# Performance work log

Hardware: AMD Instinct MI355X
Metric: run time of the kernel (lower is better)

## Reference

```python
import jax, jax.numpy as jnp
import numpy as np

T, B, I, Hd = 512, 64, 1024, 2048


def setup_inputs() -> dict:
    key = jax.random.key(0)
    ks = jax.random.split(key, 10)
    s_in = 1.0 / np.sqrt(I)
    s_h = 1.0 / np.sqrt(Hd)
    return {
        "inputs": jax.random.normal(ks[0], (T, B, I), jnp.float32),
        "state": jax.random.normal(ks[1], (B, Hd), jnp.float32),
        "W_xz": jax.random.normal(ks[2], (I, Hd), jnp.float32) * s_in,
        "W_hz": jax.random.normal(ks[3], (Hd, Hd), jnp.float32) * s_h,
        "b_z": jnp.zeros((Hd,), jnp.float32),
        "W_xr": jax.random.normal(ks[4], (I, Hd), jnp.float32) * s_in,
        "W_hr": jax.random.normal(ks[5], (Hd, Hd), jnp.float32) * s_h,
        "b_r": jnp.zeros((Hd,), jnp.float32),
        "W_xh": jax.random.normal(ks[6], (I, Hd), jnp.float32) * s_in,
        "W_hh": jax.random.normal(ks[7], (Hd, Hd), jnp.float32) * s_h,
        "b_h": jnp.zeros((Hd,), jnp.float32),
        "W_hq": jax.random.normal(ks[8], (Hd, I), jnp.float32) * s_h,
        "b_hq": jnp.zeros((I,), jnp.float32),
    }


def reference(inputs, state, W_xz, W_hz, b_z, W_xr, W_hr, b_r,
              W_xh, W_hh, b_h, W_hq, b_hq):
    def step(H, X):
        Z = jax.nn.sigmoid(X @ W_xz + H @ W_hz + b_z)
        R = jax.nn.sigmoid(X @ W_xr + H @ W_hr + b_r)
        # torch `R * H @ W_hh` parses left-to-right: (R*H) @ W_hh
        H_tilda = jnp.tanh(X @ W_xh + (R * H) @ W_hh + b_h)
        H_new = Z * H + (1.0 - Z) * H_tilda
        Y = H_new @ W_hq + b_hq
        return H_new, Y

    H_final, Ys = jax.lax.scan(step, state, inputs)  # Ys: (T, B, I)
    out = Ys.reshape(-1, Ys.shape[-1])  # torch.cat(output, dim=0) -> (T*B, I)
    return out, H_final
```

## Files before the change

### kernel.cpp

```cpp
#include <hip/hip_runtime.h>
#include <cstdint>
#include <cstddef>


#define T_ 512
#define B_ 64
#define I_ 1024
#define H_ 2048
#define NB 256
#define NTHREADS 512
#define GSTRIDE (NB * NTHREADS)

typedef __attribute__((ext_vector_type(8))) __bf16 bf16x8;
typedef __attribute__((ext_vector_type(2))) __bf16 bf16x2;
typedef __attribute__((ext_vector_type(4))) float f32x4;
typedef __attribute__((ext_vector_type(2))) float f32x2;

static constexpr unsigned SMEM_BYTES = 128 * 1024 + 20 * 1024;

static constexpr size_t OFF_SLOT = 0;
static constexpr size_t OFF_HNF  = 16384;
static constexpr size_t OFF_RHF  = 24576;
static constexpr size_t OFF_XF   = 32768;
static constexpr size_t OFF_WXZT = 36864;
static constexpr size_t SZ_WXT   = (size_t)H_ * I_ * 2;
static constexpr size_t SZ_WHT   = (size_t)H_ * H_ * 2;
static constexpr size_t OFF_WXRT = OFF_WXZT + SZ_WXT;
static constexpr size_t OFF_WXHT = OFF_WXRT + SZ_WXT;
static constexpr size_t OFF_WHZT = OFF_WXHT + SZ_WXT;
static constexpr size_t OFF_WHRT = OFF_WHZT + SZ_WHT;
static constexpr size_t OFF_WHHT = OFF_WHRT + SZ_WHT;
static constexpr size_t OFF_WHQT = OFF_WHHT + SZ_WHT;
static constexpr size_t OFF_XBF  = OFF_WHQT + SZ_WXT;
static constexpr size_t OFF_HBF  = OFF_XBF + (size_t)2 * B_ * I_ * 2;
static constexpr size_t OFF_RHBF = OFF_HBF + (size_t)2 * B_ * H_ * 2;
static constexpr size_t WS_NEEDED = OFF_RHBF + (size_t)B_ * H_ * 2;

__device__ __forceinline__ float fsigmoid(float x) { return 1.0f / (1.0f + __expf(-x)); }
__device__ __forceinline__ float ftanh(float x)    { return 2.0f / (1.0f + __expf(-2.0f * x)) - 1.0f; }

__device__ __forceinline__ void cstore8(void* p, unsigned long long v) {
    __hip_atomic_store((unsigned long long*)p, v, __ATOMIC_RELAXED, __HIP_MEMORY_SCOPE_AGENT);
}
__device__ __forceinline__ void cstore4(void* p, unsigned v) {
    __hip_atomic_store((unsigned*)p, v, __ATOMIC_RELAXED, __HIP_MEMORY_SCOPE_AGENT);
}
__device__ __forceinline__ void fstore(unsigned* p, unsigned v) {
    __hip_atomic_store(p, v, __ATOMIC_RELAXED, __HIP_MEMORY_SCOPE_AGENT);
}
__device__ __forceinline__ unsigned long long pack4bf(float a, float b, float c, float d) {
    union { unsigned short s[4]; unsigned long long u; } x;
    union { __bf16 b; unsigned short s; } t;
    t.b = (__bf16)a; x.s[0] = t.s;
    t.b = (__bf16)b; x.s[1] = t.s;
    t.b = (__bf16)c; x.s[2] = t.s;
    t.b = (__bf16)d; x.s[3] = t.s;
    return x.u;
}
__device__ __forceinline__ unsigned pack2bf(float a, float b) {
    union { unsigned short s[2]; unsigned u; } x;
    union { __bf16 b; unsigned short s; } t;
    t.b = (__bf16)a; x.s[0] = t.s;
    t.b = (__bf16)b; x.s[1] = t.s;
    return x.u;
}

template<int NFLAGS>
__device__ __forceinline__ void flag_wait(unsigned* flags, unsigned want) {
    const int tid = (int)threadIdx.x;
    if (tid < NFLAGS) {
        while (__hip_atomic_load(&flags[tid * 16], __ATOMIC_RELAXED,
                                 __HIP_MEMORY_SCOPE_AGENT) < want)
            __builtin_amdgcn_s_sleep(1);
    }
    __syncthreads();
    if (tid == 0)
        (void)__hip_atomic_load(&flags[0], __ATOMIC_ACQUIRE, __HIP_MEMORY_SCOPE_AGENT);
    __syncthreads();
    asm volatile("" ::: "memory");
}

__device__ __forceinline__ void transpose_cvt(const float* __restrict__ src,
                                              __bf16* __restrict__ dst,
                                              int K, int lgN) {
    const int N = 1 << lgN;
    const int total = K << lgN;
    for (int idx = (int)(blockIdx.x * blockDim.x + threadIdx.x); idx < total; idx += GSTRIDE) {
        int k = idx >> lgN;
        int n = idx & (N - 1);
        dst[(size_t)n * K + k] = (__bf16)src[idx];
    }
}

__device__ __forceinline__ void gload16(const void* g, void* l) {
    __builtin_amdgcn_global_load_lds(
        (const __attribute__((address_space(1))) unsigned int*)g,
        (__attribute__((address_space(3))) unsigned int*)l,
        16, 0, 0);
}

#define STAGE_SEG(i)                                                          \
    do {                                                                      \
        const int kb_ = (w + ((i) << 3)) << 5;                                \
        char* slot_ = wls + (((i) & 3) << 12);                                \
        _Pragma("unroll")                                                     \
        for (int c_ = 0; c_ < 4; ++c_) {                                      \
            const int row_ = (c_ << 4) + (lane >> 2);                         \
            const int jl_ = (lane & 3) ^ ((row_ >> 1) & 3);                   \
            gload16(A + (size_t)row_ * ks + kb_ + (jl_ << 3),                 \
                    slot_ + (c_ << 10));                                      \
        }                                                                     \
    } while (0)

#define WAITV(rem)                                                            \
    do {                                                                      \
        if ((rem) >= 3)      asm volatile("s_waitcnt vmcnt(12)" ::: "memory");\
        else if ((rem) == 2) asm volatile("s_waitcnt vmcnt(8)" ::: "memory"); \
        else if ((rem) == 1) asm volatile("s_waitcnt vmcnt(4)" ::: "memory"); \
        else                 asm volatile("s_waitcnt vmcnt(0)" ::: "memory"); \
        __builtin_amdgcn_sched_barrier(0);                                    \
    } while (0)

template<int NSEG, int OFF, int N>
__device__ __forceinline__ void gemm_lds1(
    const __bf16* __restrict__ A, int ks, const bf16x8 (&pb)[N],
    f32x4 acc[4], char* __restrict__ wls)
{
    static_assert(OFF + NSEG <= N, "frags");
    const int tid  = (int)threadIdx.x;
    const int lane = tid & 63;
    const int w    = tid >> 6;
    const int l15  = lane & 15;

    asm volatile("s_waitcnt lgkmcnt(0)" ::: "memory");
    __builtin_amdgcn_sched_barrier(0);
    STAGE_SEG(0);
    if constexpr (NSEG > 1) STAGE_SEG(1);
    if constexpr (NSEG > 2) STAGE_SEG(2);
    if constexpr (NSEG > 3) STAGE_SEG(3);
#pragma unroll
    for (int i = 0; i < NSEG; ++i) {
        WAITV(NSEG - 1 - i);
        const char* slot = wls + ((i & 3) << 12);
        bf16x8 pa[4];
#pragma unroll
        for (int m = 0; m < 4; ++m) {
            const int row = (m << 4) + l15;
            const int j   = (lane >> 4) ^ ((row >> 1) & 3);
            pa[m] = *(const bf16x8*)(slot + row * 64 + (j << 4));
        }
#pragma unroll
        for (int m = 0; m < 4; ++m)
            acc[m] = __builtin_amdgcn_mfma_f32_16x16x32_bf16(pa[m], pb[OFF + i], acc[m], 0, 0, 0);
        if (i + 4 < NSEG) {
            asm volatile("s_waitcnt lgkmcnt(0)" ::: "memory");
            __builtin_amdgcn_sched_barrier(0);
            STAGE_SEG(i + 4);
        }
    }
}

template<int N1, int N2>
__device__ __forceinline__ void gemm_lds2(
    const __bf16* __restrict__ A, int ks,
    const bf16x8 (&pb1)[N1], const bf16x8 (&pb2)[N2],
    f32x4 a1[4], f32x4 a2[4], char* __restrict__ wls)
{
    const int tid  = (int)threadIdx.x;
    const int lane = tid & 63;
    const int w    = tid >> 6;
    const int l15  = lane & 15;

    asm volatile("s_waitcnt lgkmcnt(0)" ::: "memory");
    __builtin_amdgcn_sched_barrier(0);
    STAGE_SEG(0); STAGE_SEG(1); STAGE_SEG(2); STAGE_SEG(3);
#pragma unroll
    for (int i = 0; i < 4; ++i) {
        WAITV(3 - i);
        const char* slot = wls + ((i & 3) << 12);
        bf16x8 pa[4];
#pragma unroll
        for (int m = 0; m < 4; ++m) {
            const int row = (m << 4) + l15;
            const int j   = (lane >> 4) ^ ((row >> 1) & 3);
            pa[m] = *(const bf16x8*)(slot + row * 64 + (j << 4));
        }
#pragma unroll
        for (int m = 0; m < 4; ++m) {
            a1[m] = __builtin_amdgcn_mfma_f32_16x16x32_bf16(pa[m], pb1[i], a1[m], 0, 0, 0);
            a2[m] = __builtin_amdgcn_mfma_f32_16x16x32_bf16(pa[m], pb2[i], a2[m], 0, 0, 0);
        }
    }
}

__device__ __forceinline__ void gemm_reduce(f32x4 acc[4], float* __restrict__ red,
                                            float out2[2]) {
    constexpr int RP = 20;
    const int tid  = (int)threadIdx.x;
    const int lane = tid & 63;
    const int w    = tid >> 6;
    const int l15  = lane & 15;
    const int q4   = (lane >> 4) << 2;

    if (w >= 4) {
        float* rw = red + (size_t)(w - 4) * (64 * RP);
#pragma unroll
        for (int m = 0; m < 4; ++m)
#pragma unroll
            for (int r = 0; r < 4; ++r)
                rw[((m << 4) + q4 + r) * RP + l15] = acc[m][r];
    }
    __syncthreads();
    if (w < 4) {
        float* rw = red + (size_t)w * (64 * RP);
#pragma unroll
        for (int m = 0; m < 4; ++m)
#pragma unroll
            for (int r = 0; r < 4; ++r)
                rw[((m << 4) + q4 + r) * RP + l15] += acc[m][r];
    }
    __syncthreads();
    {
        const int a = (tid >> 3) * RP + ((tid & 7) << 1);
        f32x2 s0 = *(const f32x2*)(red + a);
        f32x2 s1 = *(const f32x2*)(red + 64 * RP + a);
        f32x2 s2 = *(const f32x2*)(red + 2 * 64 * RP + a);
        f32x2 s3 = *(const f32x2*)(red + 3 * 64 * RP + a);
        f32x2 s = s0 + s1 + s2 + s3;
        out2[0] = s[0]; out2[1] = s[1];
    }
}

__global__ __launch_bounds__(NTHREADS, 2)
__attribute__((amdgpu_waves_per_eu(2, 2)))
void gru_persistent(
    const float* __restrict__ inputs, const float* __restrict__ state,
    const float* __restrict__ Wxz, const float* __restrict__ Whz, const float* __restrict__ bz,
    const float* __restrict__ Wxr, const float* __restrict__ Whr, const float* __restrict__ br,
    const float* __restrict__ Wxh, const float* __restrict__ Whh, const float* __restrict__ bh,
    const float* __restrict__ Whq, const float* __restrict__ bhq,
    float* __restrict__ out, char* __restrict__ ws) {

    unsigned* slots = (unsigned*)(ws + OFF_SLOT);
    unsigned* hnf   = (unsigned*)(ws + OFF_HNF);
    unsigned* rhf   = (unsigned*)(ws + OFF_RHF);
    unsigned* xf    = (unsigned*)(ws + OFF_XF);
    __bf16* WxzT = (__bf16*)(ws + OFF_WXZT);
    __bf16* WxrT = (__bf16*)(ws + OFF_WXRT);
    __bf16* WxhT = (__bf16*)(ws + OFF_WXHT);
    __bf16* WhzT = (__bf16*)(ws + OFF_WHZT);
    __bf16* WhrT = (__bf16*)(ws + OFF_WHRT);
    __bf16* WhhT = (__bf16*)(ws + OFF_WHHT);
    __bf16* WhqT = (__bf16*)(ws + OFF_WHQT);
    __bf16* Xbf  = (__bf16*)(ws + OFF_XBF);
    __bf16* Hbf  = (__bf16*)(ws + OFF_HBF);
    __bf16* RHbf = (__bf16*)(ws + OFF_RHBF);

    extern __shared__ char smem[];
    char* wls  = smem + ((threadIdx.x >> 6) << 14);
    float* red = (float*)(smem + 128 * 1024);

    const int b   = (int)blockIdx.x;
    const int tid = (int)threadIdx.x;
    const int c16 = (b & 127) << 4;
    const int gr  = tid >> 3;
    const int gc  = (tid & 7) << 1;

    transpose_cvt(Wxz, WxzT, I_, 11);
    transpose_cvt(Wxr, WxrT, I_, 11);
    transpose_cvt(Wxh, WxhT, I_, 11);
    transpose_cvt(Whz, WhzT, H_, 11);
    transpose_cvt(Whr, WhrT, H_, 11);
    transpose_cvt(Whh, WhhT, H_, 11);
    transpose_cvt(Whq, WhqT, H_, 10);
    {
        int q = b * NTHREADS + tid;
        if (q < B_ * I_ / 4) {
            f32x4 v = *(const f32x4*)(inputs + (size_t)q * 4);
            cstore8(Xbf + (size_t)q * 4, pack4bf(v[0], v[1], v[2], v[3]));
        }
        if (q < B_ * H_ / 4) {
            f32x4 v = *(const f32x4*)(state + (size_t)q * 4);
            cstore8(Hbf + (size_t)q * 4, pack4bf(v[0], v[1], v[2], v[3]));
        }
    }
    __syncthreads();
    __threadfence();
    if (tid == 0) fstore(&slots[b * 16], 1u);
    flag_wait<256>(slots, 1u);

    const int lane = tid & 63;
    const int w    = tid >> 6;
    const int l15  = lane & 15;
    const int q8   = (lane >> 4) << 3;

    if (b < 128) {
        bf16x8 pbA[12];
        bf16x8 pbB[12];
#pragma unroll
        for (int i = 0; i < 4; ++i)
            pbA[i] = *(const bf16x8*)(WxzT + (size_t)(c16 + l15) * I_ + ((w + (i << 3)) << 5) + q8);
#pragma unroll
        for (int i = 0; i < 8; ++i)
            pbA[4 + i] = *(const bf16x8*)(WhzT + (size_t)(c16 + l15) * H_ + ((w + (i << 3)) << 5) + q8);
#pragma unroll
        for (int i = 0; i < 4; ++i)
            pbB[i] = *(const bf16x8*)(WxhT + (size_t)(c16 + l15) * I_ + ((w + (i << 3)) << 5) + q8);
#pragma unroll
        for (int i = 0; i < 8; ++i)
            pbB[4 + i] = *(const bf16x8*)(WhhT + (size_t)(c16 + l15) * H_ + ((w + (i << 3)) << 5) + q8);

        const float bz0 = bz[c16 + gc], bz1 = bz[c16 + gc + 1];
        const float bh0 = bh[c16 + gc], bh1 = bh[c16 + gc + 1];
        float hreg[2];
        {
            f32x2 v = *(const f32x2*)(state + (size_t)gr * H_ + c16 + gc);
            hreg[0] = v[0]; hreg[1] = v[1];
        }

        f32x4 accA[4], accB[4];
#pragma unroll
        for (int m = 0; m < 4; ++m) {
            accA[m] = f32x4{0.f, 0.f, 0.f, 0.f};
            accB[m] = f32x4{0.f, 0.f, 0.f, 0.f};
        }
        gemm_lds2(Xbf, I_, pbA, pbB, accA, accB, wls);

        for (int t = 0; t < T_; ++t) {
            const int cur = t & 1, nxt = cur ^ 1;
            const __bf16* Hc = Hbf + (size_t)cur * B_ * H_;
            float o2[2];

            flag_wait<128>(hnf, (unsigned)t);
            gemm_lds1<8, 4>(Hc, H_, pbA, accA, wls);
            gemm_reduce(accA, red, o2);
            const float z0 = fsigmoid(o2[0] + bz0);
            const float z1 = fsigmoid(o2[1] + bz1);

            flag_wait<128>(rhf, (unsigned)(t + 1));
            gemm_lds1<8, 4>(RHbf, H_, pbB, accB, wls);
            gemm_reduce(accB, red, o2);
            const float ht0 = ftanh(o2[0] + bh0);
            const float ht1 = ftanh(o2[1] + bh1);
            const float hn0 = z0 * hreg[0] + (1.0f - z0) * ht0;
            const float hn1 = z1 * hreg[1] + (1.0f - z1) * ht1;
            hreg[0] = hn0; hreg[1] = hn1;
            cstore4(Hbf + (size_t)nxt * B_ * H_ + (size_t)gr * H_ + c16 + gc,
                    pack2bf(hn0, hn1));
            if (t == T_ - 1) {
                f32x2 v; v[0] = hn0; v[1] = hn1;
                *(f32x2*)(out + (size_t)T_ * B_ * I_ + (size_t)gr * H_ + c16 + gc) = v;
            }
            __syncthreads();
            if (tid == 0) {
                fstore(&hnf[b * 16], (unsigned)(t + 1));
                fstore(&slots[b * 16], (unsigned)(t + 2));
            }

#pragma unroll
            for (int m = 0; m < 4; ++m) {
                accA[m] = f32x4{0.f, 0.f, 0.f, 0.f};
                accB[m] = f32x4{0.f, 0.f, 0.f, 0.f};
            }
            if (t + 1 < T_) {
                flag_wait<64>(xf, (unsigned)(t + 1));
                gemm_lds2(Xbf + (size_t)nxt * B_ * I_, I_, pbA, pbB, accA, accB, wls);
            }
        }
    } else if (b < 192) {
        bf16x8 pbA[12];
        bf16x8 pbY[8];
#pragma unroll
        for (int i = 0; i < 4; ++i)
            pbA[i] = *(const bf16x8*)(WxrT + (size_t)(c16 + l15) * I_ + ((w + (i << 3)) << 5) + q8);
#pragma unroll
        for (int i = 0; i < 8; ++i)
            pbA[4 + i] = *(const bf16x8*)(WhrT + (size_t)(c16 + l15) * H_ + ((w + (i << 3)) << 5) + q8);
        const int yc = (b - 128) << 4;
#pragma unroll
        for (int i = 0; i < 8; ++i)
            pbY[i] = *(const bf16x8*)(WhqT + (size_t)(yc + l15) * H_ + ((w + (i << 3)) << 5) + q8);
        const float br0 = br[c16 + gc], br1 = br[c16 + gc + 1];
        const float bq0 = bhq[yc + gc], bq1 = bhq[yc + gc + 1];

        f32x4 accA[4];
#pragma unroll
        for (int m = 0; m < 4; ++m) accA[m] = f32x4{0.f, 0.f, 0.f, 0.f};
        gemm_lds1<4, 0>(Xbf, I_, pbA, accA, wls);

        for (int t = 0; t < T_; ++t) {
            const int cur = t & 1, nxt = cur ^ 1;
            const __bf16* Hc = Hbf + (size_t)cur * B_ * H_;
            float o2[2];

            flag_wait<128>(hnf, (unsigned)t);
            gemm_lds1<8, 4>(Hc, H_, pbA, accA, wls);
            gemm_reduce(accA, red, o2);
            bf16x2 h2 = *(const bf16x2*)(Hc + (size_t)gr * H_ + c16 + gc);
            const float rh0 = fsigmoid(o2[0] + br0) * (float)h2[0];
            const float rh1 = fsigmoid(o2[1] + br1) * (float)h2[1];

            flag_wait<256>(slots, (unsigned)(t + 1));
            cstore4(RHbf + (size_t)gr * H_ + c16 + gc, pack2bf(rh0, rh1));
            __syncthreads();
            if (tid == 0)
                fstore(&rhf[(b - 128) * 16], (unsigned)(t + 1));

            if (t > 0) {
                f32x4 accY[4];
#pragma unroll
                for (int m = 0; m < 4; ++m) accY[m] = f32x4{0.f, 0.f, 0.f, 0.f};
                gemm_lds1<8, 0>(Hc, H_, pbY, accY, wls);
                gemm_reduce(accY, red, o2);
                f32x2 v;
                v[0] = o2[0] + bq0;
                v[1] = o2[1] + bq1;
                *(f32x2*)(out + ((size_t)(t - 1) * B_ + gr) * I_ + yc + gc) = v;
            }
            __syncthreads();
            if (tid == 0)
                fstore(&slots[b * 16], (unsigned)(t + 2));

#pragma unroll
            for (int m = 0; m < 4; ++m) accA[m] = f32x4{0.f, 0.f, 0.f, 0.f};
            if (t + 1 < T_) {
                flag_wait<64>(xf, (unsigned)(t + 1));
                gemm_lds1<4, 0>(Xbf + (size_t)nxt * B_ * I_, I_, pbA, accA, wls);
            }
        }

        {
            flag_wait<128>(hnf, (unsigned)T_);
            f32x4 accY[4];
#pragma unroll
            for (int m = 0; m < 4; ++m) accY[m] = f32x4{0.f, 0.f, 0.f, 0.f};
            float o2[2];
            gemm_lds1<8, 0>(Hbf, H_, pbY, accY, wls);
            gemm_reduce(accY, red, o2);
            f32x2 v;
            v[0] = o2[0] + bq0;
            v[1] = o2[1] + bq1;
            *(f32x2*)(out + ((size_t)(T_ - 1) * B_ + gr) * I_ + yc + gc) = v;
        }
    } else {
        bf16x8 pbA[12];
#pragma unroll
        for (int i = 0; i < 4; ++i)
            pbA[i] = *(const bf16x8*)(WxrT + (size_t)(c16 + l15) * I_ + ((w + (i << 3)) << 5) + q8);
#pragma unroll
        for (int i = 0; i < 8; ++i)
            pbA[4 + i] = *(const bf16x8*)(WhrT + (size_t)(c16 + l15) * H_ + ((w + (i << 3)) << 5) + q8);
        const float br0 = br[c16 + gc], br1 = br[c16 + gc + 1];

        f32x4 accA[4];
#pragma unroll
        for (int m = 0; m < 4; ++m) accA[m] = f32x4{0.f, 0.f, 0.f, 0.f};
        gemm_lds1<4, 0>(Xbf, I_, pbA, accA, wls);

        for (int t = 0; t < T_; ++t) {
            const int cur = t & 1, nxt = cur ^ 1;
            const __bf16* Hc = Hbf + (size_t)cur * B_ * H_;
            float o2[2];

            flag_wait<128>(hnf, (unsigned)t);
            gemm_lds1<8, 4>(Hc, H_, pbA, accA, wls);
            gemm_reduce(accA, red, o2);
            bf16x2 h2 = *(const bf16x2*)(Hc + (size_t)gr * H_ + c16 + gc);
            const float rh0 = fsigmoid(o2[0] + br0) * (float)h2[0];
            const float rh1 = fsigmoid(o2[1] + br1) * (float)h2[1];

            flag_wait<256>(slots, (unsigned)(t + 1));
            cstore4(RHbf + (size_t)gr * H_ + c16 + gc, pack2bf(rh0, rh1));
            __syncthreads();
            if (tid == 0)
                fstore(&rhf[(b - 128) * 16], (unsigned)(t + 1));

            if (t + 1 < T_ && tid < 256) {
                const int idx = (((b - 192) << 8) + tid) << 2;
                f32x4 v = *(const f32x4*)(inputs + (size_t)(t + 1) * B_ * I_ + idx);
                cstore8(Xbf + (size_t)nxt * B_ * I_ + idx,
                        pack4bf(v[0], v[1], v[2], v[3]));
            }
            __syncthreads();
            if (tid == 0) {
                fstore(&xf[(b - 192) * 16], (unsigned)(t + 1));
                fstore(&slots[b * 16], (unsigned)(t + 2));
            }

#pragma unroll
            for (int m = 0; m < 4; ++m) accA[m] = f32x4{0.f, 0.f, 0.f, 0.f};
            if (t + 1 < T_) {
                flag_wait<64>(xf, (unsigned)(t + 1));
                gemm_lds1<4, 0>(Xbf + (size_t)nxt * B_ * I_, I_, pbA, accA, wls);
            }
        }
    }
}

extern "C" void kernel_launch(void* const* d_in, const int* in_sizes, int n_in,
                              void* d_out, int out_size, void* d_ws, size_t ws_size,
                              hipStream_t stream) {
    if (ws_size < WS_NEEDED) return;

    const float* inputs = (const float*)d_in[0];
    const float* state  = (const float*)d_in[1];
    const float* Wxz    = (const float*)d_in[2];
    const float* Whz    = (const float*)d_in[3];
    const float* bz     = (const float*)d_in[4];
    const float* Wxr    = (const float*)d_in[5];
    const float* Whr    = (const float*)d_in[6];
    const float* br     = (const float*)d_in[7];
    const float* Wxh    = (const float*)d_in[8];
    const float* Whh    = (const float*)d_in[9];
    const float* bh     = (const float*)d_in[10];
    const float* Whq    = (const float*)d_in[11];
    const float* bhq    = (const float*)d_in[12];

    static bool smem_set = false;
    if (!smem_set) {
        (void)hipFuncSetAttribute((const void*)gru_persistent,
                                  hipFuncAttributeMaxDynamicSharedMemorySize,
                                  (int)SMEM_BYTES);
        smem_set = true;
    }

    hipMemsetAsync(d_ws, 0, 36864, stream);
    gru_persistent<<<NB, NTHREADS, SMEM_BYTES, stream>>>(
        inputs, state, Wxz, Whz, bz, Wxr, Whr, br, Wxh, Whh, bh, Whq, bhq,
        (float*)d_out, (char*)d_ws);
}
```

Measured before the change: 9.007 ms.

## Fuse Z and R gate GEMMs into hidden-state blocks and rebalance block roles

Hidden-state blocks now compute the Z and R gates together with the X part of the candidate in one fused pass over shared LDS-staged X and H tiles. Each of them then writes R*H itself. Blocks 128-191 keep only the output projection and publish a new yf flag. Blocks 192-255 only convert inputs to bf16. The aim is to remove a cross-block handoff (R blocks to hidden blocks) and the slot flag barrier from the per-timestep critical path. The cost is more weight fragments held in registers per hidden block and extra waits coupling hidden updates to the Y blocks and the input converters.

```diff
diff --git a/kernel.cpp b/kernel.cpp
--- a/kernel.cpp
+++ b/kernel.cpp
@@ -22,7 +22,8 @@
 static constexpr size_t OFF_HNF  = 16384;
 static constexpr size_t OFF_RHF  = 24576;
 static constexpr size_t OFF_XF   = 32768;
-static constexpr size_t OFF_WXZT = 36864;
+static constexpr size_t OFF_YF   = 36864;
+static constexpr size_t OFF_WXZT = 40960;
 static constexpr size_t SZ_WXT   = (size_t)H_ * I_ * 2;
 static constexpr size_t SZ_WHT   = (size_t)H_ * H_ * 2;
 static constexpr size_t OFF_WXRT = OFF_WXZT + SZ_WXT;
@@ -80,6 +81,26 @@
     asm volatile("" ::: "memory");
 }
 
+template<int N1, int N2>
+__device__ __forceinline__ void flag_wait2(unsigned* f1, unsigned want1,
+                                           unsigned* f2, unsigned want2) {
+    const int tid = (int)threadIdx.x;
+    if (tid < N1) {
+        while (__hip_atomic_load(&f1[tid * 16], __ATOMIC_RELAXED,
+                                 __HIP_MEMORY_SCOPE_AGENT) < want1)
+            __builtin_amdgcn_s_sleep(1);
+    } else if (tid < N1 + N2) {
+        while (__hip_atomic_load(&f2[(tid - N1) * 16], __ATOMIC_RELAXED,
+                                 __HIP_MEMORY_SCOPE_AGENT) < want2)
+            __builtin_amdgcn_s_sleep(1);
+    }
+    __syncthreads();
+    if (tid == 0)
+        (void)__hip_atomic_load(&f1[0], __ATOMIC_ACQUIRE, __HIP_MEMORY_SCOPE_AGENT);
+    __syncthreads();
+    asm volatile("" ::: "memory");
+}
+
 __device__ __forceinline__ void transpose_cvt(const float* __restrict__ src,
                                               __bf16* __restrict__ dst,
                                               int K, int lgN) {
@@ -98,19 +119,6 @@
         (__attribute__((address_space(3))) unsigned int*)l,
         16, 0, 0);
 }
-
-#define STAGE_SEG(i)                                                          \
-    do {                                                                      \
-        const int kb_ = (w + ((i) << 3)) << 5;                                \
-        char* slot_ = wls + (((i) & 3) << 12);                                \
-        _Pragma("unroll")                                                     \
-        for (int c_ = 0; c_ < 4; ++c_) {                                      \
-            const int row_ = (c_ << 4) + (lane >> 2);                         \
-            const int jl_ = (lane & 3) ^ ((row_ >> 1) & 3);                   \
-            gload16(A + (size_t)row_ * ks + kb_ + (jl_ << 3),                 \
-                    slot_ + (c_ << 10));                                      \
-        }                                                                     \
-    } while (0)
 
 #define WAITV(rem)                                                            \
     do {                                                                      \
@@ -132,12 +140,23 @@
     const int w    = tid >> 6;
     const int l15  = lane & 15;
 
+    auto stage = [&](int i) {
+        const int kb = (w + (i << 3)) << 5;
+        char* slot = wls + ((i & 3) << 12);
+#pragma unroll
+        for (int c = 0; c < 4; ++c) {
+            const int row = (c << 4) + (lane >> 2);
+            const int j = (lane & 3) ^ ((row >> 1) & 3);
+            gload16(A + (size_t)row * ks + kb + (j << 3), slot + (c << 10));
+        }
+    };
+
     asm volatile("s_waitcnt lgkmcnt(0)" ::: "memory");
     __builtin_amdgcn_sched_barrier(0);
-    STAGE_SEG(0);
-    if constexpr (NSEG > 1) STAGE_SEG(1);
-    if constexpr (NSEG > 2) STAGE_SEG(2);
-    if constexpr (NSEG > 3) STAGE_SEG(3);
+    stage(0);
+    if constexpr (NSEG > 1) stage(1);
+    if constexpr (NSEG > 2) stage(2);
+    if constexpr (NSEG > 3) stage(3);
 #pragma unroll
     for (int i = 0; i < NSEG; ++i) {
         WAITV(NSEG - 1 - i);
@@ -155,28 +174,41 @@
         if (i + 4 < NSEG) {
             asm volatile("s_waitcnt lgkmcnt(0)" ::: "memory");
             __builtin_amdgcn_sched_barrier(0);
-            STAGE_SEG(i + 4);
-        }
-    }
-}
-
-template<int N1, int N2>
-__device__ __forceinline__ void gemm_lds2(
-    const __bf16* __restrict__ A, int ks,
-    const bf16x8 (&pb1)[N1], const bf16x8 (&pb2)[N2],
-    f32x4 a1[4], f32x4 a2[4], char* __restrict__ wls)
+            stage(i + 4);
+        }
+    }
+}
+
+__device__ __forceinline__ void gemm_fusedA(
+    const __bf16* __restrict__ Xc, const __bf16* __restrict__ Hc,
+    const bf16x8 (&pbZ)[12], const bf16x8 (&pbR)[12], const bf16x8 (&pbHx)[4],
+    f32x4 accZ[4], f32x4 accR[4], f32x4 accB[4], char* __restrict__ wls)
 {
     const int tid  = (int)threadIdx.x;
     const int lane = tid & 63;
     const int w    = tid >> 6;
     const int l15  = lane & 15;
 
+    auto stage = [&](int i) {
+        const bool isx = (i < 4);
+        const __bf16* A = isx ? Xc : Hc;
+        const int ks = isx ? I_ : H_;
+        const int kb = (isx ? (w + (i << 3)) : (w + ((i - 4) << 3))) << 5;
+        char* slot = wls + ((i & 3) << 12);
+#pragma unroll
+        for (int c = 0; c < 4; ++c) {
+            const int row = (c << 4) + (lane >> 2);
+            const int j = (lane & 3) ^ ((row >> 1) & 3);
+            gload16(A + (size_t)row * ks + kb + (j << 3), slot + (c << 10));
+        }
+    };
+
     asm volatile("s_waitcnt lgkmcnt(0)" ::: "memory");
     __builtin_amdgcn_sched_barrier(0);
-    STAGE_SEG(0); STAGE_SEG(1); STAGE_SEG(2); STAGE_SEG(3);
-#pragma unroll
-    for (int i = 0; i < 4; ++i) {
-        WAITV(3 - i);
+    stage(0); stage(1); stage(2); stage(3);
+#pragma unroll
+    for (int i = 0; i < 12; ++i) {
+        WAITV(11 - i);
         const char* slot = wls + ((i & 3) << 12);
         bf16x8 pa[4];
 #pragma unroll
@@ -186,9 +218,20 @@
             pa[m] = *(const bf16x8*)(slot + row * 64 + (j << 4));
         }
 #pragma unroll
-        for (int m = 0; m < 4; ++m) {
-            a1[m] = __builtin_amdgcn_mfma_f32_16x16x32_bf16(pa[m], pb1[i], a1[m], 0, 0, 0);
-            a2[m] = __builtin_amdgcn_mfma_f32_16x16x32_bf16(pa[m], pb2[i], a2[m], 0, 0, 0);
+        for (int m = 0; m < 4; ++m)
+            accZ[m] = __builtin_amdgcn_mfma_f32_16x16x32_bf16(pa[m], pbZ[i], accZ[m], 0, 0, 0);
+#pragma unroll
+        for (int m = 0; m < 4; ++m)
+            accR[m] = __builtin_amdgcn_mfma_f32_16x16x32_bf16(pa[m], pbR[i], accR[m], 0, 0, 0);
+        if (i < 4) {
+#pragma unroll
+            for (int m = 0; m < 4; ++m)
+                accB[m] = __builtin_amdgcn_mfma_f32_16x16x32_bf16(pa[m], pbHx[i], accB[m], 0, 0, 0);
+        }
+        if (i + 4 < 12) {
+            asm volatile("s_waitcnt lgkmcnt(0)" ::: "memory");
+            __builtin_amdgcn_sched_barrier(0);
+            stage(i + 4);
         }
     }
 }
@@ -245,6 +288,7 @@
     unsigned* hnf   = (unsigned*)(ws + OFF_HNF);
     unsigned* rhf   = (unsigned*)(ws + OFF_RHF);
     unsigned* xf    = (unsigned*)(ws + OFF_XF);
+    unsigned* yf    = (unsigned*)(ws + OFF_YF);
     __bf16* WxzT = (__bf16*)(ws + OFF_WXZT);
     __bf16* WxrT = (__bf16*)(ws + OFF_WXRT);
     __bf16* WxhT = (__bf16*)(ws + OFF_WXHT);
@@ -262,7 +306,6 @@
 
     const int b   = (int)blockIdx.x;
     const int tid = (int)threadIdx.x;
-    const int c16 = (b & 127) << 4;
     const int gr  = tid >> 3;
     const int gc  = (tid & 7) << 1;
 
@@ -295,22 +338,32 @@
     const int q8   = (lane >> 4) << 3;
 
     if (b < 128) {
-        bf16x8 pbA[12];
-        bf16x8 pbB[12];
+        const int c16 = b << 4;
+        bf16x8 pbZ[12];
+        bf16x8 pbR[12];
+        bf16x8 pbHx[4];
+        bf16x8 pbHh[8];
 #pragma unroll
         for (int i = 0; i < 4; ++i)
-            pbA[i] = *(const bf16x8*)(WxzT + (size_t)(c16 + l15) * I_ + ((w + (i << 3)) << 5) + q8);
+            pbZ[i] = *(const bf16x8*)(WxzT + (size_t)(c16 + l15) * I_ + ((w + (i << 3)) << 5) + q8);
 #pragma unroll
         for (int i = 0; i < 8; ++i)
-            pbA[4 + i] = *(const bf16x8*)(WhzT + (size_t)(c16 + l15) * H_ + ((w + (i << 3)) << 5) + q8);
+            pbZ[4 + i] = *(const bf16x8*)(WhzT + (size_t)(c16 + l15) * H_ + ((w + (i << 3)) << 5) + q8);
 #pragma unroll
         for (int i = 0; i < 4; ++i)
-            pbB[i] = *(const bf16x8*)(WxhT + (size_t)(c16 + l15) * I_ + ((w + (i << 3)) << 5) + q8);
+            pbR[i] = *(const bf16x8*)(WxrT + (size_t)(c16 + l15) * I_ + ((w + (i << 3)) << 5) + q8);
 #pragma unroll
         for (int i = 0; i < 8; ++i)
-            pbB[4 + i] = *(const bf16x8*)(WhhT + (size_t)(c16 + l15) * H_ + ((w + (i << 3)) << 5) + q8);
+            pbR[4 + i] = *(const bf16x8*)(WhrT + (size_t)(c16 + l15) * H_ + ((w + (i << 3)) << 5) + q8);
+#pragma unroll
+        for (int i = 0; i < 4; ++i)
+            pbHx[i] = *(const bf16x8*)(WxhT + (size_t)(c16 + l15) * I_ + ((w + (i << 3)) << 5) + q8);
+#pragma unroll
+        for (int i = 0; i < 8; ++i)
+            pbHh[i] = *(const bf16x8*)(WhhT + (size_t)(c16 + l15) * H_ + ((w + (i << 3)) << 5) + q8);
 
         const float bz0 = bz[c16 + gc], bz1 = bz[c16 + gc + 1];
+        const float br0 = br[c16 + gc], br1 = br[c16 + gc + 1];
         const float bh0 = bh[c16 + gc], bh1 = bh[c16 + gc + 1];
         float hreg[2];
         {
@@ -318,27 +371,37 @@
             hreg[0] = v[0]; hreg[1] = v[1];
         }
 
-        f32x4 accA[4], accB[4];
-#pragma unroll
-        for (int m = 0; m < 4; ++m) {
-            accA[m] = f32x4{0.f, 0.f, 0.f, 0.f};
-            accB[m] = f32x4{0.f, 0.f, 0.f, 0.f};
-        }
-        gemm_lds2(Xbf, I_, pbA, pbB, accA, accB, wls);
-
         for (int t = 0; t < T_; ++t) {
             const int cur = t & 1, nxt = cur ^ 1;
+            const __bf16* Xc = Xbf + (size_t)cur * B_ * I_;
             const __bf16* Hc = Hbf + (size_t)cur * B_ * H_;
             float o2[2];
 
-            flag_wait<128>(hnf, (unsigned)t);
-            gemm_lds1<8, 4>(Hc, H_, pbA, accA, wls);
-            gemm_reduce(accA, red, o2);
+            flag_wait2<128, 64>(hnf, (unsigned)t, xf, (unsigned)t);
+
+            f32x4 accZ[4], accR[4], accB[4];
+#pragma unroll
+            for (int m = 0; m < 4; ++m) {
+                accZ[m] = f32x4{0.f, 0.f, 0.f, 0.f};
+                accR[m] = f32x4{0.f, 0.f, 0.f, 0.f};
+                accB[m] = f32x4{0.f, 0.f, 0.f, 0.f};
+            }
+            gemm_fusedA(Xc, Hc, pbZ, pbR, pbHx, accZ, accR, accB, wls);
+            gemm_reduce(accZ, red, o2);
             const float z0 = fsigmoid(o2[0] + bz0);
             const float z1 = fsigmoid(o2[1] + bz1);
-
-            flag_wait<128>(rhf, (unsigned)(t + 1));
-            gemm_lds1<8, 4>(RHbf, H_, pbB, accB, wls);
+            __syncthreads();
+            gemm_reduce(accR, red, o2);
+            bf16x2 h2 = *(const bf16x2*)(Hc + (size_t)gr * H_ + c16 + gc);
+            const float rh0 = fsigmoid(o2[0] + br0) * (float)h2[0];
+            const float rh1 = fsigmoid(o2[1] + br1) * (float)h2[1];
+            cstore4(RHbf + (size_t)gr * H_ + c16 + gc, pack2bf(rh0, rh1));
+            __syncthreads();
+            if (tid == 0) fstore(&rhf[b * 16], (unsigned)(t + 1));
+
+            flag_wait2<128, 64>(rhf, (unsigned)(t + 1), yf, (unsigned)t);
+
+            gemm_lds1<8, 0>(RHbf, H_, pbHh, accB, wls);
             gemm_reduce(accB, red, o2);
             const float ht0 = ftanh(o2[0] + bh0);
             const float ht1 = ftanh(o2[1] + bh1);
@@ -352,64 +415,24 @@
                 *(f32x2*)(out + (size_t)T_ * B_ * I_ + (size_t)gr * H_ + c16 + gc) = v;
             }
             __syncthreads();
-            if (tid == 0) {
-                fstore(&hnf[b * 16], (unsigned)(t + 1));
-                fstore(&slots[b * 16], (unsigned)(t + 2));
-            }
-
-#pragma unroll
-            for (int m = 0; m < 4; ++m) {
-                accA[m] = f32x4{0.f, 0.f, 0.f, 0.f};
-                accB[m] = f32x4{0.f, 0.f, 0.f, 0.f};
-            }
-            if (t + 1 < T_) {
-                flag_wait<64>(xf, (unsigned)(t + 1));
-                gemm_lds2(Xbf + (size_t)nxt * B_ * I_, I_, pbA, pbB, accA, accB, wls);
-            }
+            if (tid == 0) fstore(&hnf[b * 16], (unsigned)(t + 1));
         }
     } else if (b < 192) {
-        bf16x8 pbA[12];
+        const int yc = (b - 128) << 4;
         bf16x8 pbY[8];
-#pragma unroll
-        for (int i = 0; i < 4; ++i)
-            pbA[i] = *(const bf16x8*)(WxrT + (size_t)(c16 + l15) * I_ + ((w + (i << 3)) << 5) + q8);
-#pragma unroll
-        for (int i = 0; i < 8; ++i)
-            pbA[4 + i] = *(const bf16x8*)(WhrT + (size_t)(c16 + l15) * H_ + ((w + (i << 3)) << 5) + q8);
-        const int yc = (b - 128) << 4;
 #pragma unroll
         for (int i = 0; i < 8; ++i)
             pbY[i] = *(const bf16x8*)(WhqT + (size_t)(yc + l15) * H_ + ((w + (i << 3)) << 5) + q8);
-        const float br0 = br[c16 + gc], br1 = br[c16 + gc + 1];
         const float bq0 = bhq[yc + gc], bq1 = bhq[yc + gc + 1];
 
-        f32x4 accA[4];
-#pragma unroll
-        for (int m = 0; m < 4; ++m) accA[m] = f32x4{0.f, 0.f, 0.f, 0.f};
-        gemm_lds1<4, 0>(Xbf, I_, pbA, accA, wls);
-
         for (int t = 0; t < T_; ++t) {
-            const int cur = t & 1, nxt = cur ^ 1;
-            const __bf16* Hc = Hbf + (size_t)cur * B_ * H_;
-            float o2[2];
-
+            const __bf16* Hc = Hbf + (size_t)(t & 1) * B_ * H_;
             flag_wait<128>(hnf, (unsigned)t);
-            gemm_lds1<8, 4>(Hc, H_, pbA, accA, wls);
-            gemm_reduce(accA, red, o2);
-            bf16x2 h2 = *(const bf16x2*)(Hc + (size_t)gr * H_ + c16 + gc);
-            const float rh0 = fsigmoid(o2[0] + br0) * (float)h2[0];
-            const float rh1 = fsigmoid(o2[1] + br1) * (float)h2[1];
-
-            flag_wait<256>(slots, (unsigned)(t + 1));
-            cstore4(RHbf + (size_t)gr * H_ + c16 + gc, pack2bf(rh0, rh1));
-            __syncthreads();
-            if (tid == 0)
-                fstore(&rhf[(b - 128) * 16], (unsigned)(t + 1));
-
             if (t > 0) {
                 f32x4 accY[4];
 #pragma unroll
                 for (int m = 0; m < 4; ++m) accY[m] = f32x4{0.f, 0.f, 0.f, 0.f};
+                float o2[2];
                 gemm_lds1<8, 0>(Hc, H_, pbY, accY, wls);
                 gemm_reduce(accY, red, o2);
                 f32x2 v;
@@ -417,16 +440,7 @@
                 v[1] = o2[1] + bq1;
                 *(f32x2*)(out + ((size_t)(t - 1) * B_ + gr) * I_ + yc + gc) = v;
             }
-            __syncthreads();
-            if (tid == 0)
-                fstore(&slots[b * 16], (unsigned)(t + 2));
-
-#pragma unroll
-            for (int m = 0; m < 4; ++m) accA[m] = f32x4{0.f, 0.f, 0.f, 0.f};
-            if (t + 1 < T_) {
-                flag_wait<64>(xf, (unsigned)(t + 1));
-                gemm_lds1<4, 0>(Xbf + (size_t)nxt * B_ * I_, I_, pbA, accA, wls);
-            }
+            if (tid == 0) fstore(&yf[(b - 128) * 16], (unsigned)(t + 1));
         }
 
         {
@@ -443,56 +457,17 @@
             *(f32x2*)(out + ((size_t)(T_ - 1) * B_ + gr) * I_ + yc + gc) = v;
         }
     } else {
-        bf16x8 pbA[12];
-#pragma unroll
-        for (int i = 0; i < 4; ++i)
-            pbA[i] = *(const bf16x8*)(WxrT + (size_t)(c16 + l15) * I_ + ((w + (i << 3)) << 5) + q8);
-#pragma unroll
-        for (int i = 0; i < 8; ++i)
-            pbA[4 + i] = *(const bf16x8*)(WhrT + (size_t)(c16 + l15) * H_ + ((w + (i << 3)) << 5) + q8);
-        const float br0 = br[c16 + gc], br1 = br[c16 + gc + 1];
-
-        f32x4 accA[4];
-#pragma unroll
-        for (int m = 0; m < 4; ++m) accA[m] = f32x4{0.f, 0.f, 0.f, 0.f};
-        gemm_lds1<4, 0>(Xbf, I_, pbA, accA, wls);
-
-        for (int t = 0; t < T_; ++t) {
-            const int cur = t & 1, nxt = cur ^ 1;
-            const __bf16* Hc = Hbf + (size_t)cur * B_ * H_;
-            float o2[2];
-
-            flag_wait<128>(hnf, (unsigned)t);
-            gemm_lds1<8, 4>(Hc, H_, pbA, accA, wls);
-            gemm_reduce(accA, red, o2);
-            bf16x2 h2 = *(const bf16x2*)(Hc + (size_t)gr * H_ + c16 + gc);
-            const float rh0 = fsigmoid(o2[0] + br0) * (float)h2[0];
-            const float rh1 = fsigmoid(o2[1] + br1) * (float)h2[1];
-
-            flag_wait<256>(slots, (unsigned)(t + 1));
-            cstore4(RHbf + (size_t)gr * H_ + c16 + gc, pack2bf(rh0, rh1));
-            __syncthreads();
-            if (tid == 0)
-                fstore(&rhf[(b - 128) * 16], (unsigned)(t + 1));
-
-            if (t + 1 < T_ && tid < 256) {
+        for (int t = 0; t + 1 < T_; ++t) {
+            const int nxt = (t & 1) ^ 1;
+            flag_wait<128>(rhf, (unsigned)t);
+            if (tid < 256) {
                 const int idx = (((b - 192) << 8) + tid) << 2;
                 f32x4 v = *(const f32x4*)(inputs + (size_t)(t + 1) * B_ * I_ + idx);
                 cstore8(Xbf + (size_t)nxt * B_ * I_ + idx,
                         pack4bf(v[0], v[1], v[2], v[3]));
             }
             __syncthreads();
-            if (tid == 0) {
-                fstore(&xf[(b - 192) * 16], (unsigned)(t + 1));
-                fstore(&slots[b * 16], (unsigned)(t + 2));
-            }
-
-#pragma unroll
-            for (int m = 0; m < 4; ++m) accA[m] = f32x4{0.f, 0.f, 0.f, 0.f};
-            if (t + 1 < T_) {
-                flag_wait<64>(xf, (unsigned)(t + 1));
-                gemm_lds1<4, 0>(Xbf + (size_t)nxt * B_ * I_, I_, pbA, accA, wls);
-            }
+            if (tid == 0) fstore(&xf[(b - 192) * 16], (unsigned)(t + 1));
         }
     }
 }
@@ -524,7 +499,7 @@
         smem_set = true;
     }
 
-    hipMemsetAsync(d_ws, 0, 36864, stream);
+    hipMemsetAsync(d_ws, 0, 40960, stream);
     gru_persistent<<<NB, NTHREADS, SMEM_BYTES, stream>>>(
         inputs, state, Wxz, Whz, bz, Wxr, Whr, br, Wxh, Whh, bh, Whq, bhq,
         (float*)d_out, (char*)d_ws);
```

Result: slower. 12.81 ms (+42.2%).
